# Optimization experiments

Measured on AMD Instinct MI355X. Metric: run time of the kernel, lower is better.

Reference implementation:

```python
import jax, jax.numpy as jnp
import numpy as np

B, S, D = 4, 8192, 512


def log_g(x):
    # torch: where(x>=0, log(relu(x)+0.5), -softplus(-x)); relu(x)+0.5 >= 0.5 so log is safe
    return jnp.where(x >= 0, jnp.log(jax.nn.relu(x) + 0.5), -jax.nn.softplus(-x))


def parallel_scan_log(log_coeffs, log_values):
    # log_coeffs: (B,S,D); log_values: (B,S+1,D)
    a_star = jnp.pad(jnp.cumsum(log_coeffs, axis=1), ((0, 0), (1, 0), (0, 0)))  # (B,S+1,D)
    log_h = a_star + jax.lax.cumlogsumexp(log_values - a_star, axis=1)
    return jnp.exp(log_h)[:, 1:]  # (B,S,D)


def setup_inputs() -> dict:
    key = jax.random.key(0)
    ks = jax.random.split(key, 7)
    scale = 1.0 / np.sqrt(D)
    x = jax.random.normal(ks[0], (B, S, D), dtype=jnp.float32)
    pre_h = jnp.zeros((B, 1, D), dtype=jnp.float32)
    Wf = jax.random.normal(ks[1], (D, D), dtype=jnp.float32) * scale
    bf = jax.random.normal(ks[2], (D,), dtype=jnp.float32) * 0.01
    Wi = jax.random.normal(ks[3], (D, D), dtype=jnp.float32) * scale
    bi = jax.random.normal(ks[4], (D,), dtype=jnp.float32) * 0.01
    Wh = jax.random.normal(ks[5], (D, D), dtype=jnp.float32) * scale
    bh = jax.random.normal(ks[6], (D,), dtype=jnp.float32) * 0.01
    return {"x": x, "pre_h": pre_h, "Wf": Wf, "bf": bf, "Wi": Wi, "bi": bi, "Wh": Wh, "bh": bh}


def reference(x, pre_h, Wf, bf, Wi, bi, Wh, bh):
    # gates: log(sigmoid(k)) = -softplus(-k)
    log_f = -jax.nn.softplus(-(jnp.einsum('bsd,de->bse', x, Wf) + bf))
    log_i = -jax.nn.softplus(-(jnp.einsum('bsd,de->bse', x, Wi) + bi))
    log_tilde_h = log_g(jnp.einsum('bsd,de->bse', x, Wh) + bh)
    log_pre_h = log_g(pre_h)  # (B,1,D)
    log_values = jnp.concatenate([log_pre_h, log_i + log_tilde_h], axis=1)  # (B,S+1,D)
    return parallel_scan_log(log_f, log_values)
```

## Files before the change

### kernel.cpp

```cpp
#include <hip/hip_runtime.h>
#include <hip/hip_bf16.h>

#define BATCH 4
#define SEQ   8192
#define DIM   512
#define DD    (DIM*DIM)
#define M_TOT (BATCH*SEQ)
#define NCHUNK 128
#define CLEN   64

typedef __attribute__((ext_vector_type(4))) int int4v;
typedef __attribute__((ext_vector_type(8))) unsigned short ushort8v;

__device__ __forceinline__ float sigmoidf_(float x) {
    return 1.0f / (1.0f + __expf(-x));
}
__device__ __forceinline__ float gfun_(float x) {
    return (x >= 0.0f) ? (x + 0.5f) : sigmoidf_(x);
}

__device__ __forceinline__ void stage16(const void* g, void* lds) {
    __builtin_amdgcn_global_load_lds((const __attribute__((address_space(1))) void*)g,
                                     (__attribute__((address_space(3))) void*)lds,
                                     16, 0, 0);
}

__global__ __launch_bounds__(256) void quant_x(const float* __restrict__ x,
                                               char* __restrict__ xh, char* __restrict__ xl)
{
    const int t = blockIdx.x * 256 + threadIdx.x;
    float4 v = ((const float4*)x)[t];
    float vals[4] = {v.x, v.y, v.z, v.w};
    char hs[4], ls[4];
    #pragma unroll
    for (int e = 0; e < 4; ++e) {
        float c = fminf(fmaxf(vals[e], -15.8f), 15.8f);
        int q = (int)rintf(c * 2048.0f);
        int hi = (q + 128) >> 8;
        int lo = q - (hi << 8);
        hs[e] = (char)hi; ls[e] = (char)lo;
    }
    char4 hv = {hs[0], hs[1], hs[2], hs[3]};
    char4 lv = {ls[0], ls[1], ls[2], ls[3]};
    *(char4*)&xh[(size_t)t * 4] = hv;
    *(char4*)&xl[(size_t)t * 4] = lv;
}

__global__ __launch_bounds__(256) void quant_wT(
    const float* __restrict__ Wf, const float* __restrict__ Wi, const float* __restrict__ Wh,
    char* __restrict__ wth, char* __restrict__ wtl)
{
    __shared__ float tile[64][65];
    const int g = blockIdx.z;
    const float* W = (g == 0) ? Wf : (g == 1) ? Wi : Wh;
    const int k0 = blockIdx.x * 64, n0 = blockIdx.y * 64;
    const int c = threadIdx.x & 63, r4 = threadIdx.x >> 6;
    #pragma unroll
    for (int p = 0; p < 16; ++p) {
        int r = p * 4 + r4;
        tile[r][c] = W[(size_t)(k0 + r) * DIM + n0 + c];
    }
    __syncthreads();
    const size_t gbase = (size_t)g * DD;
    #pragma unroll
    for (int p = 0; p < 16; ++p) {
        int nr = p * 4 + r4;
        float w = tile[c][nr];
        float cl = fminf(fmaxf(w, -0.49f), 0.49f);
        int q = (int)rintf(cl * 65536.0f);
        int hi = (q + 128) >> 8;
        int lo = q - (hi << 8);
        size_t o = gbase + (size_t)(n0 + nr) * DIM + k0 + c;
        wth[o] = (char)hi;
        wtl[o] = (char)lo;
    }
}

__global__ __launch_bounds__(512, 4) void gemm_f(
    const char* __restrict__ xh, const char* __restrict__ xl,
    const char* __restrict__ wth, const char* __restrict__ wtl,
    const float* __restrict__ bfv, float* __restrict__ fb)
{
    __shared__ char smem[65536];
    char (*sA)[2][128][64] = (char (*)[2][128][64])smem;
    char (*sB)[2][128][64] = (char (*)[2][128][64])(smem + 32768);

    const int bid = blockIdx.x;
    const int xr  = bid & 7;
    const int t   = bid >> 3;
    const int mmt = t >> 2;
    const int n0  = (t & 3) * 128;
    const int m0  = (xr + (mmt << 3)) * 128;

    const int tid  = threadIdx.x;
    const int wave = tid >> 6;
    const int lane = tid & 63;
    const int wi = wave >> 2, wj = wave & 3;

    const int smm  = tid >> 2;
    const int skb  = (tid & 3) * 16;
    const int sksw = skb ^ (((smm >> 1) & 3) << 4);
    const int swrow = (tid >> 6) * 16;
    const char* gx_h = xh  + (size_t)(m0 + smm) * DIM + sksw;
    const char* gx_l = xl  + (size_t)(m0 + smm) * DIM + sksw;
    const char* gw_h = wth + (size_t)(n0 + smm) * DIM + sksw;
    const char* gw_l = wtl + (size_t)(n0 + smm) * DIM + sksw;

    int4v P2[4][2], P1[4][2];
    const int4v zero = {0, 0, 0, 0};
    #pragma unroll
    for (int i = 0; i < 4; ++i)
        #pragma unroll
        for (int j = 0; j < 2; ++j) { P2[i][j] = zero; P1[i][j] = zero; }

    stage16(gx_h, &sA[0][0][swrow][0]);
    stage16(gx_l, &sA[0][1][swrow][0]);
    stage16(gw_h, &sB[0][0][swrow][0]);
    stage16(gw_l, &sB[0][1][swrow][0]);

    #pragma unroll
    for (int kt = 0; kt < 8; ++kt) {
        const int cur = kt & 1;
        if (kt < 7) {
            const int nb = cur ^ 1;
            const int ko = (kt + 1) * 64;
            stage16(gx_h + ko, &sA[nb][0][swrow][0]);
            stage16(gx_l + ko, &sA[nb][1][swrow][0]);
            stage16(gw_h + ko, &sB[nb][0][swrow][0]);
            stage16(gw_l + ko, &sB[nb][1][swrow][0]);
            asm volatile("s_waitcnt vmcnt(4)" ::: "memory");
        } else {
            asm volatile("s_waitcnt vmcnt(0)" ::: "memory");
        }
        asm volatile("s_barrier" ::: "memory");

        const int kseg = (lane >> 4) * 16;
        int4v bhf[2], blf[2];
        #pragma unroll
        for (int j = 0; j < 2; ++j) {
            const int col = wj * 32 + j * 16 + (lane & 15);
            const int ks  = kseg ^ (((col >> 1) & 3) << 4);
            bhf[j] = *(const int4v*)&sB[cur][0][col][ks];
            blf[j] = *(const int4v*)&sB[cur][1][col][ks];
        }
        __builtin_amdgcn_s_setprio(1);
        #pragma unroll
        for (int i = 0; i < 4; ++i) {
            const int row = wi * 64 + i * 16 + (lane & 15);
            const int ks  = kseg ^ (((row >> 1) & 3) << 4);
            int4v ahf = *(const int4v*)&sA[cur][0][row][ks];
            int4v alf = *(const int4v*)&sA[cur][1][row][ks];
            #pragma unroll
            for (int j = 0; j < 2; ++j) {
                P2[i][j] = __builtin_amdgcn_mfma_i32_16x16x64_i8(ahf, bhf[j], P2[i][j], 0, 0, 0);
                P1[i][j] = __builtin_amdgcn_mfma_i32_16x16x64_i8(ahf, blf[j], P1[i][j], 0, 0, 0);
                P1[i][j] = __builtin_amdgcn_mfma_i32_16x16x64_i8(alf, bhf[j], P1[i][j], 0, 0, 0);
            }
        }
        __builtin_amdgcn_s_setprio(0);
        asm volatile("s_barrier" ::: "memory");
    }

    const float c2 = 1.0f / 2048.0f;
    const float c1 = 1.0f / 524288.0f;
    #pragma unroll
    for (int j = 0; j < 2; ++j) {
        const int col = n0 + wj * 32 + j * 16 + (lane & 15);
        const float bv = bfv[col];
        #pragma unroll
        for (int i = 0; i < 4; ++i) {
            #pragma unroll
            for (int r = 0; r < 4; ++r) {
                const float kv = (float)P2[i][j][r] * c2 + (float)P1[i][j][r] * c1 + bv;
                const int row = m0 + wi * 64 + i * 16 + (lane >> 4) * 4 + r;
                fb[(size_t)row * DIM + col] = sigmoidf_(kv);
            }
        }
    }
}

__global__ __launch_bounds__(512, 2) void gemm_ih(
    const char* __restrict__ xh, const char* __restrict__ xl,
    const char* __restrict__ wth, const char* __restrict__ wtl,
    const float* __restrict__ biv, const float* __restrict__ bhv,
    unsigned short* __restrict__ vb)
{
    extern __shared__ char smem[];
    char (*sA)[2][128][64]    = (char (*)[2][128][64])smem;
    char (*sB)[2][2][128][64] = (char (*)[2][2][128][64])(smem + 32768);
    unsigned short (*lds16)[136] = (unsigned short (*)[136])smem;

    const int bid = blockIdx.x;
    const int xr  = bid & 7;
    const int t   = bid >> 3;
    const int mmt = t >> 2;
    const int n0  = (t & 3) * 128;
    const int m0  = (xr + (mmt << 3)) * 128;

    const int tid  = threadIdx.x;
    const int wave = tid >> 6;
    const int lane = tid & 63;
    const int wi = wave >> 2, wj = wave & 3;

    const int smm  = tid >> 2;
    const int skb  = (tid & 3) * 16;
    const int sksw = skb ^ (((smm >> 1) & 3) << 4);
    const int swrow = (tid >> 6) * 16;
    const char* gx_h  = xh  + (size_t)(m0 + smm) * DIM + sksw;
    const char* gx_l  = xl  + (size_t)(m0 + smm) * DIM + sksw;
    const char* gwi_h = wth + (size_t)1 * DD + (size_t)(n0 + smm) * DIM + sksw;
    const char* gwi_l = wtl + (size_t)1 * DD + (size_t)(n0 + smm) * DIM + sksw;
    const char* gwh_h = wth + (size_t)2 * DD + (size_t)(n0 + smm) * DIM + sksw;
    const char* gwh_l = wtl + (size_t)2 * DD + (size_t)(n0 + smm) * DIM + sksw;

    int4v Pi2[4][2], Pi1[4][2], Ph2[4][2], Ph1[4][2];
    const int4v zero = {0, 0, 0, 0};
    #pragma unroll
    for (int i = 0; i < 4; ++i)
        #pragma unroll
        for (int j = 0; j < 2; ++j) {
            Pi2[i][j] = zero; Pi1[i][j] = zero;
            Ph2[i][j] = zero; Ph1[i][j] = zero;
        }

    stage16(gx_h,  &sA[0][0][swrow][0]);
    stage16(gx_l,  &sA[0][1][swrow][0]);
    stage16(gwi_h, &sB[0][0][0][swrow][0]);
    stage16(gwi_l, &sB[0][0][1][swrow][0]);
    stage16(gwh_h, &sB[0][1][0][swrow][0]);
    stage16(gwh_l, &sB[0][1][1][swrow][0]);

    #pragma unroll
    for (int kt = 0; kt < 8; ++kt) {
        const int cur = kt & 1;
        if (kt < 7) {
            const int nb = cur ^ 1;
            const int ko = (kt + 1) * 64;
            stage16(gx_h  + ko, &sA[nb][0][swrow][0]);
            stage16(gx_l  + ko, &sA[nb][1][swrow][0]);
            stage16(gwi_h + ko, &sB[nb][0][0][swrow][0]);
            stage16(gwi_l + ko, &sB[nb][0][1][swrow][0]);
            stage16(gwh_h + ko, &sB[nb][1][0][swrow][0]);
            stage16(gwh_l + ko, &sB[nb][1][1][swrow][0]);
            asm volatile("s_waitcnt vmcnt(6)" ::: "memory");
        } else {
            asm volatile("s_waitcnt vmcnt(0)" ::: "memory");
        }
        asm volatile("s_barrier" ::: "memory");

        const int kseg = (lane >> 4) * 16;
        int4v bih[2], bil[2], bhh[2], bhl[2];
        #pragma unroll
        for (int j = 0; j < 2; ++j) {
            const int col = wj * 32 + j * 16 + (lane & 15);
            const int ks  = kseg ^ (((col >> 1) & 3) << 4);
            bih[j] = *(const int4v*)&sB[cur][0][0][col][ks];
            bil[j] = *(const int4v*)&sB[cur][0][1][col][ks];
            bhh[j] = *(const int4v*)&sB[cur][1][0][col][ks];
            bhl[j] = *(const int4v*)&sB[cur][1][1][col][ks];
        }
        __builtin_amdgcn_s_setprio(1);
        #pragma unroll
        for (int i = 0; i < 4; ++i) {
            const int row = wi * 64 + i * 16 + (lane & 15);
            const int ks  = kseg ^ (((row >> 1) & 3) << 4);
            int4v ahf = *(const int4v*)&sA[cur][0][row][ks];
            int4v alf = *(const int4v*)&sA[cur][1][row][ks];
            #pragma unroll
            for (int j = 0; j < 2; ++j) {
                Pi2[i][j] = __builtin_amdgcn_mfma_i32_16x16x64_i8(ahf, bih[j], Pi2[i][j], 0, 0, 0);
                Pi1[i][j] = __builtin_amdgcn_mfma_i32_16x16x64_i8(ahf, bil[j], Pi1[i][j], 0, 0, 0);
                Pi1[i][j] = __builtin_amdgcn_mfma_i32_16x16x64_i8(alf, bih[j], Pi1[i][j], 0, 0, 0);
                Ph2[i][j] = __builtin_amdgcn_mfma_i32_16x16x64_i8(ahf, bhh[j], Ph2[i][j], 0, 0, 0);
                Ph1[i][j] = __builtin_amdgcn_mfma_i32_16x16x64_i8(ahf, bhl[j], Ph1[i][j], 0, 0, 0);
                Ph1[i][j] = __builtin_amdgcn_mfma_i32_16x16x64_i8(alf, bhh[j], Ph1[i][j], 0, 0, 0);
            }
        }
        __builtin_amdgcn_s_setprio(0);
        asm volatile("s_barrier" ::: "memory");
    }

    const float c2 = 1.0f / 2048.0f;
    const float c1 = 1.0f / 524288.0f;
    #pragma unroll
    for (int j = 0; j < 2; ++j) {
        const int lc = wj * 32 + j * 16 + (lane & 15);
        const float bvi = biv[n0 + lc];
        const float bvh = bhv[n0 + lc];
        #pragma unroll
        for (int i = 0; i < 4; ++i) {
            #pragma unroll
            for (int r = 0; r < 4; ++r) {
                const float ki = (float)Pi2[i][j][r] * c2 + (float)Pi1[i][j][r] * c1 + bvi;
                const float kh = (float)Ph2[i][j][r] * c2 + (float)Ph1[i][j][r] * c1 + bvh;
                const float v  = sigmoidf_(ki) * gfun_(kh);
                const int lr = wi * 64 + i * 16 + (lane >> 4) * 4 + r;
                lds16[lr][lc] = (unsigned short)fminf(rintf(v * 8192.0f), 65535.0f);
            }
        }
    }
    __syncthreads();
    const int r  = tid >> 2;
    const int cq = tid & 3;
    #pragma unroll
    for (int it = 0; it < 4; ++it) {
        const int ci = cq + it * 4;
        ushort8v vv = *(const ushort8v*)&lds16[r][ci * 8];
        *(ushort8v*)&vb[(size_t)(m0 + r) * DIM + n0 + ci * 8] = vv;
    }
}

#define VSCALE (1.0f / 8192.0f)

__global__ __launch_bounds__(256) void scan_pass1(
    const float* __restrict__ fb, const unsigned short* __restrict__ vb,
    float* __restrict__ Ach, float* __restrict__ Bch)
{
    const int dq  = threadIdx.x & 127;
    const int sub = threadIdx.x >> 7;
    const int c = blockIdx.x * 2 + sub;
    const int b = blockIdx.y;
    const int d = dq * 4;
    float A[4] = {1.f, 1.f, 1.f, 1.f};
    float B[4] = {0.f, 0.f, 0.f, 0.f};
    size_t base = ((size_t)(b * SEQ + c * CLEN)) * DIM + d;
    #pragma unroll 4
    for (int t = 0; t < CLEN; ++t) {
        float4  f4 = *(const float4*)&fb[base + (size_t)t * DIM];
        ushort4 v4 = *(const ushort4*)&vb[base + (size_t)t * DIM];
        float f[4] = {f4.x, f4.y, f4.z, f4.w};
        float v[4] = {(float)v4.x * VSCALE, (float)v4.y * VSCALE,
                      (float)v4.z * VSCALE, (float)v4.w * VSCALE};
        #pragma unroll
        for (int e = 0; e < 4; ++e) { B[e] = fmaf(f[e], B[e], v[e]); A[e] *= f[e]; }
    }
    const size_t idx = (size_t)(b * NCHUNK + c) * DIM + d;
    *(float4*)&Ach[idx] = *(float4*)A;
    *(float4*)&Bch[idx] = *(float4*)B;
}

__global__ __launch_bounds__(64) void scan_pass2(
    const float* __restrict__ pre_h,
    const float* __restrict__ Ach, const float* __restrict__ Bch,
    float* __restrict__ carry)
{
    const int gidx = blockIdx.x * 64 + threadIdx.x;
    const int b = gidx >> 9;
    const int d = gidx & (DIM - 1);
    float h = gfun_(pre_h[b * DIM + d]);
    #pragma unroll 4
    for (int c = 0; c < NCHUNK; ++c) {
        const int idx = (b * NCHUNK + c) * DIM + d;
        carry[idx] = h;
        h = fmaf(Ach[idx], h, Bch[idx]);
    }
}

__global__ __launch_bounds__(256) void scan_pass3(
    const float* __restrict__ fb, const unsigned short* __restrict__ vb,
    const float* __restrict__ carry, float* __restrict__ out)
{
    const int dq  = threadIdx.x & 127;
    const int sub = threadIdx.x >> 7;
    const int c = blockIdx.x * 2 + sub;
    const int b = blockIdx.y;
    const int d = dq * 4;
    float4 h4 = *(const float4*)&carry[(size_t)(b * NCHUNK + c) * DIM + d];
    float h[4] = {h4.x, h4.y, h4.z, h4.w};
    size_t base = ((size_t)(b * SEQ + c * CLEN)) * DIM + d;
    #pragma unroll 4
    for (int t = 0; t < CLEN; ++t) {
        float4  f4 = *(const float4*)&fb[base + (size_t)t * DIM];
        ushort4 v4 = *(const ushort4*)&vb[base + (size_t)t * DIM];
        float f[4] = {f4.x, f4.y, f4.z, f4.w};
        float v[4] = {(float)v4.x * VSCALE, (float)v4.y * VSCALE,
                      (float)v4.z * VSCALE, (float)v4.w * VSCALE};
        float o[4];
        #pragma unroll
        for (int e = 0; e < 4; ++e) { h[e] = fmaf(f[e], h[e], v[e]); o[e] = h[e]; }
        *(float4*)&out[base + (size_t)t * DIM] = *(float4*)o;
    }
}

extern "C" void kernel_launch(void* const* d_in, const int* in_sizes, int n_in,
                              void* d_out, int out_size, void* d_ws, size_t ws_size,
                              hipStream_t stream) {
    const float* x     = (const float*)d_in[0];
    const float* pre_h = (const float*)d_in[1];
    const float* Wf    = (const float*)d_in[2];
    const float* bf    = (const float*)d_in[3];
    const float* Wi    = (const float*)d_in[4];
    const float* bi    = (const float*)d_in[5];
    const float* Wh    = (const float*)d_in[6];
    const float* bh    = (const float*)d_in[7];
    float* out = (float*)d_out;

    char* ws = (char*)d_ws;
    const size_t XQ = (size_t)M_TOT * DIM;
    const size_t WQ = (size_t)3 * DD;
    const size_t FB = (size_t)M_TOT * DIM * sizeof(float);
    const size_t VB = (size_t)M_TOT * DIM * 2;
    const size_t CH = (size_t)BATCH * NCHUNK * DIM * sizeof(float);

    char*  xh  = ws;
    char*  xl  = ws + XQ;
    char*  wth = ws + 2 * XQ;
    char*  wtl = ws + 2 * XQ + WQ;
    float* fbuf = (float*)(ws + 2 * XQ + 2 * WQ);
    unsigned short* vbuf = (unsigned short*)((char*)fbuf + FB);
    float* Ach   = (float*)((char*)vbuf + VB);
    float* Bch   = (float*)((char*)Ach + CH);
    float* carry = (float*)((char*)Bch + CH);

    static bool attr_set = false;
    if (!attr_set) {
        hipFuncSetAttribute((const void*)gemm_ih,
                            hipFuncAttributeMaxDynamicSharedMemorySize, 98304);
        attr_set = true;
    }

    quant_x<<<(M_TOT * DIM / 4) / 256, 256, 0, stream>>>(x, xh, xl);
    quant_wT<<<dim3(8, 8, 3), 256, 0, stream>>>(Wf, Wi, Wh, wth, wtl);
    gemm_f<<<1024, 512, 0, stream>>>(xh, xl, wth, wtl, bf, fbuf);
    gemm_ih<<<1024, 512, 98304, stream>>>(xh, xl, wth, wtl, bi, bh, vbuf);
    scan_pass1<<<dim3(NCHUNK / 2, BATCH), 256, 0, stream>>>(fbuf, vbuf, Ach, Bch);
    scan_pass2<<<32, 64, 0, stream>>>(pre_h, Ach, Bch, carry);
    scan_pass3<<<dim3(NCHUNK / 2, BATCH), 256, 0, stream>>>(fbuf, vbuf, carry, out);
}
```

Before: 302.9 us.

## Fuse three scan passes into one kernel with last-block carry propagation

New measurement: 386.5 us. 1.28x slower.

```diff
diff --git a/kernel.cpp b/kernel.cpp
--- a/kernel.cpp
+++ b/kernel.cpp
@@ -8,9 +8,11 @@
 #define M_TOT (BATCH*SEQ)
 #define NCHUNK 128
 #define CLEN   64
+#define NBLK_PER_B (NCHUNK/2)
 
 typedef __attribute__((ext_vector_type(4))) int int4v;
 typedef __attribute__((ext_vector_type(8))) unsigned short ushort8v;
+typedef __attribute__((ext_vector_type(4))) float f4v;
 
 __device__ __forceinline__ float sigmoidf_(float x) {
     return 1.0f / (1.0f + __expf(-x));
@@ -312,18 +314,24 @@
 
 #define VSCALE (1.0f / 8192.0f)
 
-__global__ __launch_bounds__(256) void scan_pass1(
+__global__ __launch_bounds__(256) void scan_fused(
     const float* __restrict__ fb, const unsigned short* __restrict__ vb,
-    float* __restrict__ Ach, float* __restrict__ Bch)
+    const float* __restrict__ pre_h,
+    float* __restrict__ Ach, float* __restrict__ Bch,
+    float* __restrict__ carry, unsigned* sync,
+    float* __restrict__ out)
 {
     const int dq  = threadIdx.x & 127;
     const int sub = threadIdx.x >> 7;
     const int c = blockIdx.x * 2 + sub;
     const int b = blockIdx.y;
     const int d = dq * 4;
+    unsigned* flags = sync;
+    unsigned* cnt   = sync + (size_t)BATCH * NCHUNK * 32;
+
     float A[4] = {1.f, 1.f, 1.f, 1.f};
     float B[4] = {0.f, 0.f, 0.f, 0.f};
-    size_t base = ((size_t)(b * SEQ + c * CLEN)) * DIM + d;
+    const size_t base = ((size_t)(b * SEQ + c * CLEN)) * DIM + d;
     #pragma unroll 4
     for (int t = 0; t < CLEN; ++t) {
         float4  f4 = *(const float4*)&fb[base + (size_t)t * DIM];
@@ -337,37 +345,46 @@
     const size_t idx = (size_t)(b * NCHUNK + c) * DIM + d;
     *(float4*)&Ach[idx] = *(float4*)A;
     *(float4*)&Bch[idx] = *(float4*)B;
-}
-
-__global__ __launch_bounds__(64) void scan_pass2(
-    const float* __restrict__ pre_h,
-    const float* __restrict__ Ach, const float* __restrict__ Bch,
-    float* __restrict__ carry)
-{
-    const int gidx = blockIdx.x * 64 + threadIdx.x;
-    const int b = gidx >> 9;
-    const int d = gidx & (DIM - 1);
-    float h = gfun_(pre_h[b * DIM + d]);
-    #pragma unroll 4
-    for (int c = 0; c < NCHUNK; ++c) {
-        const int idx = (b * NCHUNK + c) * DIM + d;
-        carry[idx] = h;
-        h = fmaf(Ach[idx], h, Bch[idx]);
-    }
-}
-
-__global__ __launch_bounds__(256) void scan_pass3(
-    const float* __restrict__ fb, const unsigned short* __restrict__ vb,
-    const float* __restrict__ carry, float* __restrict__ out)
-{
-    const int dq  = threadIdx.x & 127;
-    const int sub = threadIdx.x >> 7;
-    const int c = blockIdx.x * 2 + sub;
-    const int b = blockIdx.y;
-    const int d = dq * 4;
-    float4 h4 = *(const float4*)&carry[(size_t)(b * NCHUNK + c) * DIM + d];
+
+    __threadfence();
+    __shared__ int fin;
+    if (threadIdx.x == 0) {
+        unsigned old = __hip_atomic_fetch_add(&cnt[b], 1u,
+                          __ATOMIC_ACQ_REL, __HIP_MEMORY_SCOPE_AGENT);
+        fin = (old == NBLK_PER_B - 1);
+    }
+    __syncthreads();
+
+    if (fin) {
+        __threadfence();
+        const int dd = threadIdx.x * 2;
+        float h0 = gfun_(pre_h[b * DIM + dd]);
+        float h1 = gfun_(pre_h[b * DIM + dd + 1]);
+        for (int cg = 0; cg < NCHUNK; cg += 16) {
+            #pragma unroll 4
+            for (int cc = cg; cc < cg + 16; ++cc) {
+                const size_t ix = (size_t)(b * NCHUNK + cc) * DIM + dd;
+                carry[ix]     = h0;
+                carry[ix + 1] = h1;
+                float2 a2 = *(const float2*)&Ach[ix];
+                float2 b2 = *(const float2*)&Bch[ix];
+                h0 = fmaf(a2.x, h0, b2.x);
+                h1 = fmaf(a2.y, h1, b2.y);
+            }
+            __syncthreads();
+            if (threadIdx.x < 16) {
+                __hip_atomic_store(&flags[(size_t)(b * NCHUNK + cg + threadIdx.x) * 32],
+                                   1u, __ATOMIC_RELEASE, __HIP_MEMORY_SCOPE_AGENT);
+            }
+        }
+    }
+
+    unsigned* myflag = &flags[(size_t)(b * NCHUNK + c) * 32];
+    while (__hip_atomic_load(myflag, __ATOMIC_ACQUIRE, __HIP_MEMORY_SCOPE_AGENT) == 0u)
+        __builtin_amdgcn_s_sleep(8);
+
+    float4 h4 = *(const float4*)&carry[idx];
     float h[4] = {h4.x, h4.y, h4.z, h4.w};
-    size_t base = ((size_t)(b * SEQ + c * CLEN)) * DIM + d;
     #pragma unroll 4
     for (int t = 0; t < CLEN; ++t) {
         float4  f4 = *(const float4*)&fb[base + (size_t)t * DIM];
@@ -375,10 +392,10 @@
         float f[4] = {f4.x, f4.y, f4.z, f4.w};
         float v[4] = {(float)v4.x * VSCALE, (float)v4.y * VSCALE,
                       (float)v4.z * VSCALE, (float)v4.w * VSCALE};
-        float o[4];
+        f4v o;
         #pragma unroll
         for (int e = 0; e < 4; ++e) { h[e] = fmaf(f[e], h[e], v[e]); o[e] = h[e]; }
-        *(float4*)&out[base + (size_t)t * DIM] = *(float4*)o;
+        __builtin_nontemporal_store(o, (f4v*)&out[base + (size_t)t * DIM]);
     }
 }
 
@@ -401,6 +418,7 @@
     const size_t FB = (size_t)M_TOT * DIM * sizeof(float);
     const size_t VB = (size_t)M_TOT * DIM * 2;
     const size_t CH = (size_t)BATCH * NCHUNK * DIM * sizeof(float);
+    const size_t SYNC = (size_t)BATCH * NCHUNK * 32 * 4 + BATCH * 4;
 
     char*  xh  = ws;
     char*  xl  = ws + XQ;
@@ -411,6 +429,7 @@
     float* Ach   = (float*)((char*)vbuf + VB);
     float* Bch   = (float*)((char*)Ach + CH);
     float* carry = (float*)((char*)Bch + CH);
+    unsigned* syncbuf = (unsigned*)((char*)carry + CH);
 
     static bool attr_set = false;
     if (!attr_set) {
@@ -419,11 +438,11 @@
         attr_set = true;
     }
 
+    hipMemsetAsync(syncbuf, 0, SYNC, stream);
     quant_x<<<(M_TOT * DIM / 4) / 256, 256, 0, stream>>>(x, xh, xl);
     quant_wT<<<dim3(8, 8, 3), 256, 0, stream>>>(Wf, Wi, Wh, wth, wtl);
     gemm_f<<<1024, 512, 0, stream>>>(xh, xl, wth, wtl, bf, fbuf);
     gemm_ih<<<1024, 512, 98304, stream>>>(xh, xl, wth, wtl, bi, bh, vbuf);
-    scan_pass1<<<dim3(NCHUNK / 2, BATCH), 256, 0, stream>>>(fbuf, vbuf, Ach, Bch);
-    scan_pass2<<<32, 64, 0, stream>>>(pre_h, Ach, Bch, carry);
-    scan_pass3<<<dim3(NCHUNK / 2, BATCH), 256, 0, stream>>>(fbuf, vbuf, carry, out);
-}
+    scan_fused<<<dim3(NCHUNK / 2, BATCH), 256, 0, stream>>>(
+        fbuf, vbuf, pre_h, Ach, Bch, carry, syncbuf, out);
+}
```

## Use finer scan chunks with a parallel block-level carry scan and nontemporal output stores

Applied to the files above, without the earlier changes.

Result: faster. 278.9 us (-7.9%).

```diff
diff --git a/kernel.cpp b/kernel.cpp
--- a/kernel.cpp
+++ b/kernel.cpp
@@ -6,11 +6,13 @@
 #define DIM   512
 #define DD    (DIM*DIM)
 #define M_TOT (BATCH*SEQ)
-#define NCHUNK 128
-#define CLEN   64
+#define NCHUNK 512
+#define CLEN   16
+#define NSEG   32
 
 typedef __attribute__((ext_vector_type(4))) int int4v;
 typedef __attribute__((ext_vector_type(8))) unsigned short ushort8v;
+typedef __attribute__((ext_vector_type(4))) float f4v;
 
 __device__ __forceinline__ float sigmoidf_(float x) {
     return 1.0f / (1.0f + __expf(-x));
@@ -339,20 +341,58 @@
     *(float4*)&Bch[idx] = *(float4*)B;
 }
 
-__global__ __launch_bounds__(64) void scan_pass2(
+__global__ __launch_bounds__(1024) void scan_pass2(
     const float* __restrict__ pre_h,
     const float* __restrict__ Ach, const float* __restrict__ Bch,
     float* __restrict__ carry)
 {
-    const int gidx = blockIdx.x * 64 + threadIdx.x;
-    const int b = gidx >> 9;
-    const int d = gidx & (DIM - 1);
-    float h = gfun_(pre_h[b * DIM + d]);
+    __shared__ float As[NSEG][33], Bs[NSEG][33];
+    const int b    = blockIdx.y;
+    const int dgrp = blockIdx.x;
+    const int seg  = threadIdx.x >> 5;
+    const int dl   = threadIdx.x & 31;
+    const int d    = dgrp * 32 + dl;
+    const int c0   = seg * 16;
+
+    float A = 1.0f, Bv = 0.0f;
     #pragma unroll 4
-    for (int c = 0; c < NCHUNK; ++c) {
-        const int idx = (b * NCHUNK + c) * DIM + d;
-        carry[idx] = h;
-        h = fmaf(Ach[idx], h, Bch[idx]);
+    for (int cc = 0; cc < 16; ++cc) {
+        const size_t ix = (size_t)(b * NCHUNK + c0 + cc) * DIM + d;
+        const float a  = Ach[ix];
+        const float bb = Bch[ix];
+        Bv = fmaf(a, Bv, bb);
+        A *= a;
+    }
+    As[seg][dl] = A;
+    Bs[seg][dl] = Bv;
+    __syncthreads();
+
+    float Ai = A, Bi = Bv;
+    #pragma unroll
+    for (int s = 1; s < NSEG; s <<= 1) {
+        float Al = 1.0f, Bl = 0.0f;
+        const bool act = (seg >= s);
+        if (act) { Al = As[seg - s][dl]; Bl = Bs[seg - s][dl]; }
+        __syncthreads();
+        if (act) {
+            Bi = fmaf(Ai, Bl, Bi);
+            Ai = Ai * Al;
+            As[seg][dl] = Ai;
+            Bs[seg][dl] = Bi;
+        }
+        __syncthreads();
+    }
+
+    const float h0 = gfun_(pre_h[b * DIM + d]);
+    float h;
+    if (seg == 0) h = h0;
+    else          h = fmaf(As[seg - 1][dl], h0, Bs[seg - 1][dl]);
+
+    #pragma unroll 4
+    for (int cc = 0; cc < 16; ++cc) {
+        const size_t ix = (size_t)(b * NCHUNK + c0 + cc) * DIM + d;
+        carry[ix] = h;
+        h = fmaf(Ach[ix], h, Bch[ix]);
     }
 }
 
@@ -375,10 +415,10 @@
         float f[4] = {f4.x, f4.y, f4.z, f4.w};
         float v[4] = {(float)v4.x * VSCALE, (float)v4.y * VSCALE,
                       (float)v4.z * VSCALE, (float)v4.w * VSCALE};
-        float o[4];
+        f4v o;
         #pragma unroll
         for (int e = 0; e < 4; ++e) { h[e] = fmaf(f[e], h[e], v[e]); o[e] = h[e]; }
-        *(float4*)&out[base + (size_t)t * DIM] = *(float4*)o;
+        __builtin_nontemporal_store(o, (f4v*)&out[base + (size_t)t * DIM]);
     }
 }
 
@@ -424,6 +464,6 @@
     gemm_f<<<1024, 512, 0, stream>>>(xh, xl, wth, wtl, bf, fbuf);
     gemm_ih<<<1024, 512, 98304, stream>>>(xh, xl, wth, wtl, bi, bh, vbuf);
     scan_pass1<<<dim3(NCHUNK / 2, BATCH), 256, 0, stream>>>(fbuf, vbuf, Ach, Bch);
-    scan_pass2<<<32, 64, 0, stream>>>(pre_h, Ach, Bch, carry);
+    scan_pass2<<<dim3(DIM / 32, BATCH), 1024, 0, stream>>>(pre_h, Ach, Bch, carry);
     scan_pass3<<<dim3(NCHUNK / 2, BATCH), 256, 0, stream>>>(fbuf, vbuf, carry, out);
 }
```
